# Kernel optimization log

Hardware: AMD Instinct MI355X
Metric: run time of the kernel (lower is better)

Reference implementation:

```python
import jax, jax.numpy as jnp
import numpy as np

B, L, S, H, E, D = 2, 2048, 2048, 8, 64, 64

def setup_inputs() -> dict:
    key = jax.random.key(0)
    kq, kk, kv = jax.random.split(key, 3)
    queries = jax.random.normal(kq, (B, L, H, E), dtype=jnp.float32)
    keys = jax.random.normal(kk, (B, S, H, E), dtype=jnp.float32)
    values = jax.random.normal(kv, (B, S, H, D), dtype=jnp.float32)
    return {"queries": queries, "keys": keys, "values": values}

def reference(queries, keys, values):
    # queries: [B,L,H,E], keys: [B,S,H,E], values: [B,S,H,D]
    E_ = queries.shape[-1]
    scale = 1.0 / jnp.sqrt(jnp.asarray(E_, dtype=queries.dtype))
    # scores: [B,H,L,S]
    scores = jnp.einsum('blhe,bshe->bhls', queries, keys)
    # mask_flag=False, use_relative_pos=False, dropout=0.0 -> identity
    A = jax.nn.softmax(scale * scores, axis=-1)
    # output: [B,L,H,D]
    V = jnp.einsum('bhls,bshd->blhd', A, values)
    return V
```

## Files before the change

kernel.cpp:

```cpp
#include <hip/hip_runtime.h>
#include <hip/hip_bf16.h>


#define LOG2E 1.44269504088896340736f
#define SCL2 0.18033688011112042f

#if __has_builtin(__builtin_amdgcn_exp2f)
#define EXP2(x) __builtin_amdgcn_exp2f(x)
#else
#define EXP2(x) exp2f(x)
#endif

typedef __attribute__((ext_vector_type(8))) short bf16x8;
typedef __attribute__((ext_vector_type(4))) float f32x4;
typedef __attribute__((ext_vector_type(16))) float f32x16;

static constexpr int Bc = 2, Lc = 2048, Sc = 2048, Hc = 8, Ec = 64, Dc = 64;
static constexpr int BH = Bc * Hc;
static constexpr int ELEMS = Bc * Lc * Hc * Ec;

static __device__ __forceinline__ unsigned short bfb(float x) {
  union { __hip_bfloat16 h; unsigned short u; } c;
  c.h = __float2bfloat16(x);
  return c.u;
}
static __device__ __forceinline__ unsigned pkbf(float a, float b) {
  union { __hip_bfloat162 h; unsigned u; } c;
  c.h = __float22bfloat162_rn(make_float2(a, b));
  return c.u;
}
static __device__ __forceinline__ bf16x8 pack4(unsigned w0, unsigned w1,
                                               unsigned w2, unsigned w3) {
  union { unsigned u[4]; bf16x8 v; } c;
  c.u[0] = w0; c.u[1] = w1; c.u[2] = w2; c.u[3] = w3;
  return c.v;
}

static __device__ __forceinline__ void plswap(unsigned a, unsigned b,
                                              unsigned& o0, unsigned& o1, int hi) {
#if __has_builtin(__builtin_amdgcn_permlane32_swap)
  auto r = __builtin_amdgcn_permlane32_swap(a, b, false, false);
  o0 = r[0];
  o1 = r[1];
#else
  unsigned ax = (unsigned)__shfl_xor((int)a, 32);
  unsigned bx = (unsigned)__shfl_xor((int)b, 32);
  o0 = hi ? bx : a;
  o1 = hi ? b : ax;
#endif
}
static __device__ __forceinline__ float cross_half_max(float x, int hi) {
  unsigned ua, ub;
  plswap(__float_as_uint(x), __float_as_uint(x), ua, ub, hi);
  return fmaxf(__uint_as_float(ua), __uint_as_float(ub));
}
static __device__ __forceinline__ float cross_half_sum(float x, int hi) {
  unsigned ua, ub;
  plswap(__float_as_uint(x), __float_as_uint(x), ua, ub, hi);
  return __uint_as_float(ua) + __uint_as_float(ub);
}

__global__ __launch_bounds__(256) void prep_kv_kernel(const float* __restrict__ K,
                                                      const float* __restrict__ V,
                                                      __hip_bfloat16* __restrict__ Kc,
                                                      __hip_bfloat16* __restrict__ Vt) {
  __shared__ __hip_bfloat16 tile[4][64][68];
  if (blockIdx.x < 1024) {
    int t = blockIdx.x * 256 + threadIdx.x;
    int f = t * 8;
    int e = f & 63;
    int h = (f >> 6) & 7;
    int s = (f >> 9) & 2047;
    int b = f >> 20;
    float4 v0 = *reinterpret_cast<const float4*>(K + f);
    float4 v1 = *reinterpret_cast<const float4*>(K + f + 4);
    int es = e >> 4, hi = (e >> 3) & 1;
    int kb = s >> 5, qi = s & 31;
    int o = ((b << 3) + h) * (Sc * 64) + kb * 2048 + es * 512 + hi * 256 + qi * 8;
    union { ushort u[8]; uint4 q; } pk;
    pk.u[0] = bfb(v0.x); pk.u[1] = bfb(v0.y); pk.u[2] = bfb(v0.z); pk.u[3] = bfb(v0.w);
    pk.u[4] = bfb(v1.x); pk.u[5] = bfb(v1.y); pk.u[6] = bfb(v1.z); pk.u[7] = bfb(v1.w);
    *reinterpret_cast<uint4*>(Kc + o) = pk.q;
  } else {
    const int w = threadIdx.x >> 6;
    const int lane = threadIdx.x & 63;
    const int task = (blockIdx.x - 1024) * 4 + w;
    const int st = task & 31;
    const int bh = task >> 5;
    const int s0 = st * 64;
    const int b = bh >> 3, h = bh & 7;
#pragma unroll 4
    for (int j = 0; j < 64; ++j) {
      float v = V[((b * Sc + s0 + j) * Hc + h) * 64 + lane];
      tile[w][j][lane] = __float2bfloat16(v);
    }
    __syncthreads();
    const int qi = lane & 31, hi = lane >> 5;
    __hip_bfloat16* Vb = Vt + bh * (Sc * 64);
#pragma unroll
    for (int kb2 = 0; kb2 < 2; ++kb2)
#pragma unroll
      for (int d0 = 0; d0 < 2; ++d0)
#pragma unroll
        for (int ks = 0; ks < 2; ++ks) {
          union { ushort u[8]; uint4 q; } pk;
#pragma unroll
          for (int j = 0; j < 8; ++j) {
            union { __hip_bfloat16 h; ushort u; } c;
            c.h = tile[w][kb2 * 32 + ks * 16 + hi * 8 + j][d0 * 32 + qi];
            pk.u[j] = c.u;
          }
          int o = ((s0 >> 5) + kb2) * 2048 + d0 * 1024 + ks * 512 + lane * 8;
          *reinterpret_cast<uint4*>(Vb + o) = pk.q;
        }
  }
}

static __device__ __forceinline__ void sm_group(f32x16& sc, float& m, float& l,
                                                f32x16& oA, f32x16& oB, int hi,
                                                bf16x8& pb0, bf16x8& pb1) {
  float x0 = fmaxf(fmaxf(sc[0], sc[1]), fmaxf(sc[2], sc[3]));
  float x1 = fmaxf(fmaxf(sc[4], sc[5]), fmaxf(sc[6], sc[7]));
  float x2 = fmaxf(fmaxf(sc[8], sc[9]), fmaxf(sc[10], sc[11]));
  float x3 = fmaxf(fmaxf(sc[12], sc[13]), fmaxf(sc[14], sc[15]));
  float mx = fmaxf(fmaxf(x0, x1), fmaxf(x2, x3));

  if (__any(mx > m + 64.0f)) {
    float mrow = cross_half_max(mx, hi);
    float mnew = fmaxf(m, mrow);
    float corr = EXP2((m - mnew) * SCL2);
    l *= corr;
#pragma unroll
    for (int r = 0; r < 16; ++r) { oA[r] *= corr; oB[r] *= corr; }
    m = mnew;
  }
  float mL = m * SCL2;
#pragma unroll
  for (int r = 0; r < 16; ++r) sc[r] = EXP2(sc[r] * SCL2 - mL);

  float r0 = (sc[0] + sc[1]) + (sc[2] + sc[3]);
  float r1 = (sc[4] + sc[5]) + (sc[6] + sc[7]);
  float r2 = (sc[8] + sc[9]) + (sc[10] + sc[11]);
  float r3 = (sc[12] + sc[13]) + (sc[14] + sc[15]);
  l += (r0 + r1) + (r2 + r3);

  unsigned c0, c1, c2, c3, y0, y1, y2, y3;
  c0 = pkbf(sc[0], sc[1]);  c1 = pkbf(sc[4], sc[5]);
  c2 = pkbf(sc[2], sc[3]);  c3 = pkbf(sc[6], sc[7]);
  plswap(c0, c1, y0, y2, hi);
  plswap(c2, c3, y1, y3, hi);
  pb0 = pack4(y0, y1, y2, y3);
  c0 = pkbf(sc[8], sc[9]);   c1 = pkbf(sc[12], sc[13]);
  c2 = pkbf(sc[10], sc[11]); c3 = pkbf(sc[14], sc[15]);
  plswap(c0, c1, y0, y2, hi);
  plswap(c2, c3, y1, y3, hi);
  pb1 = pack4(y0, y1, y2, y3);
}

__global__ __launch_bounds__(256, 2) void attn_kernel(const float* __restrict__ Qf,
                                                      const __hip_bfloat16* __restrict__ Kc,
                                                      const __hip_bfloat16* __restrict__ Vt,
                                                      float* __restrict__ Out) {
  __shared__ float obuf[4][2][16][64];
  __shared__ float mlb[2][4][2][32];

  const int lid = blockIdx.x;
  const int xcd = lid & 7;
  const int i = lid >> 3;
  const int bh = (xcd << 1) | (i >> 5);
  const int q0 = (i & 31) << 6;
  const int w = threadIdx.x >> 6;
  const int lane = threadIdx.x & 63;
  const int qi = lane & 31;
  const int hi = lane >> 5;
  const int b = bh >> 3, h = bh & 7;

  const __hip_bfloat16* Kh = Kc + bh * (Sc * 64);
  const __hip_bfloat16* Vh = Vt + bh * (Sc * 64);

  bf16x8 qf[2][4];
#pragma unroll
  for (int g = 0; g < 2; ++g) {
    const float* qrow = Qf + ((b * Lc + q0 + g * 32 + qi) * Hc + h) * 64 + hi * 8;
#pragma unroll
    for (int es = 0; es < 4; ++es) {
      float4 a = *reinterpret_cast<const float4*>(qrow + es * 16);
      float4 c = *reinterpret_cast<const float4*>(qrow + es * 16 + 4);
      qf[g][es] = pack4(pkbf(a.x, a.y), pkbf(a.z, a.w), pkbf(c.x, c.y), pkbf(c.z, c.w));
    }
  }

  f32x16 zero;
#pragma unroll
  for (int r = 0; r < 16; ++r) zero[r] = 0.f;

  f32x16 oa0 = zero, ob0 = zero, oa1 = zero, ob1 = zero;
  float m0 = -1.0e30f, l0 = 0.f, m1 = -1.0e30f, l1 = 0.f;

  bf16x8 kA0, kA1, kA2, kA3, vA0, vA1, vA2, vA3;
  bf16x8 kB0, kB1, kB2, kB3, vB0, vB1, vB2, vB3;

  auto loadKV = [&](bf16x8& k0, bf16x8& k1, bf16x8& k2, bf16x8& k3,
                    bf16x8& v0, bf16x8& v1, bf16x8& v2, bf16x8& v3, int s) {
    const __hip_bfloat16* Kp = Kh + (s >> 5) * 2048 + lane * 8;
    k0 = *reinterpret_cast<const bf16x8*>(Kp + 0 * 512);
    k1 = *reinterpret_cast<const bf16x8*>(Kp + 1 * 512);
    k2 = *reinterpret_cast<const bf16x8*>(Kp + 2 * 512);
    k3 = *reinterpret_cast<const bf16x8*>(Kp + 3 * 512);
    const __hip_bfloat16* Vp = Vh + (s >> 5) * 2048 + lane * 8;
    v0 = *reinterpret_cast<const bf16x8*>(Vp + 0 * 512);
    v1 = *reinterpret_cast<const bf16x8*>(Vp + 1 * 512);
    v2 = *reinterpret_cast<const bf16x8*>(Vp + 2 * 512);
    v3 = *reinterpret_cast<const bf16x8*>(Vp + 3 * 512);
  };

  auto compute = [&](bf16x8 k0, bf16x8 k1, bf16x8 k2, bf16x8 k3,
                     bf16x8 v0, bf16x8 v1, bf16x8 v2, bf16x8 v3) {
    f32x16 sc0, sc1;
    __builtin_amdgcn_s_setprio(1);
    sc0 = __builtin_amdgcn_mfma_f32_32x32x16_bf16(k0, qf[0][0], zero, 0, 0, 0);
    sc0 = __builtin_amdgcn_mfma_f32_32x32x16_bf16(k1, qf[0][1], sc0, 0, 0, 0);
    sc0 = __builtin_amdgcn_mfma_f32_32x32x16_bf16(k2, qf[0][2], sc0, 0, 0, 0);
    sc0 = __builtin_amdgcn_mfma_f32_32x32x16_bf16(k3, qf[0][3], sc0, 0, 0, 0);
    sc1 = __builtin_amdgcn_mfma_f32_32x32x16_bf16(k0, qf[1][0], zero, 0, 0, 0);
    sc1 = __builtin_amdgcn_mfma_f32_32x32x16_bf16(k1, qf[1][1], sc1, 0, 0, 0);
    sc1 = __builtin_amdgcn_mfma_f32_32x32x16_bf16(k2, qf[1][2], sc1, 0, 0, 0);
    sc1 = __builtin_amdgcn_mfma_f32_32x32x16_bf16(k3, qf[1][3], sc1, 0, 0, 0);
    __builtin_amdgcn_s_setprio(0);

    bf16x8 pb0, pb1;
    sm_group(sc0, m0, l0, oa0, ob0, hi, pb0, pb1);
    __builtin_amdgcn_s_setprio(1);
    oa0 = __builtin_amdgcn_mfma_f32_32x32x16_bf16(v0, pb0, oa0, 0, 0, 0);
    oa0 = __builtin_amdgcn_mfma_f32_32x32x16_bf16(v1, pb1, oa0, 0, 0, 0);
    ob0 = __builtin_amdgcn_mfma_f32_32x32x16_bf16(v2, pb0, ob0, 0, 0, 0);
    ob0 = __builtin_amdgcn_mfma_f32_32x32x16_bf16(v3, pb1, ob0, 0, 0, 0);
    __builtin_amdgcn_s_setprio(0);

    sm_group(sc1, m1, l1, oa1, ob1, hi, pb0, pb1);
    __builtin_amdgcn_s_setprio(1);
    oa1 = __builtin_amdgcn_mfma_f32_32x32x16_bf16(v0, pb0, oa1, 0, 0, 0);
    oa1 = __builtin_amdgcn_mfma_f32_32x32x16_bf16(v1, pb1, oa1, 0, 0, 0);
    ob1 = __builtin_amdgcn_mfma_f32_32x32x16_bf16(v2, pb0, ob1, 0, 0, 0);
    ob1 = __builtin_amdgcn_mfma_f32_32x32x16_bf16(v3, pb1, ob1, 0, 0, 0);
    __builtin_amdgcn_s_setprio(0);
  };

  loadKV(kA0, kA1, kA2, kA3, vA0, vA1, vA2, vA3, w * 32);
  for (int s = w * 32; s < Sc; s += 256) {
    loadKV(kB0, kB1, kB2, kB3, vB0, vB1, vB2, vB3, s + 128);
    compute(kA0, kA1, kA2, kA3, vA0, vA1, vA2, vA3);
    if (s + 256 < Sc)
      loadKV(kA0, kA1, kA2, kA3, vA0, vA1, vA2, vA3, s + 256);
    compute(kB0, kB1, kB2, kB3, vB0, vB1, vB2, vB3);
  }

  l0 = cross_half_sum(l0, hi);
  l1 = cross_half_sum(l1, hi);

  if (hi == 0) {
    mlb[0][w][0][qi] = m0; mlb[0][w][1][qi] = l0;
    mlb[1][w][0][qi] = m1; mlb[1][w][1][qi] = l1;
  }
  __syncthreads();
  float myf[2], inv[2];
#pragma unroll
  for (int g = 0; g < 2; ++g) {
    float mm = fmaxf(fmaxf(mlb[g][0][0][qi], mlb[g][1][0][qi]),
                     fmaxf(mlb[g][2][0][qi], mlb[g][3][0][qi]));
    float Lt = 0.f;
#pragma unroll
    for (int sw = 0; sw < 4; ++sw)
      Lt += EXP2((mlb[g][sw][0][qi] - mm) * SCL2) * mlb[g][sw][1][qi];
    float mreg = g ? m1 : m0;
    myf[g] = EXP2((mreg - mm) * SCL2);
    inv[g] = 1.0f / Lt;
  }
  const int d0 = w >> 1, rr = (w & 1) * 8;
#pragma unroll
  for (int g = 0; g < 2; ++g) {
    if (g) __syncthreads();
    const f32x16& A = g ? oa1 : oa0;
    const f32x16& Bv = g ? ob1 : ob0;
#pragma unroll
    for (int r = 0; r < 16; ++r) {
      obuf[w][0][r][lane] = A[r] * myf[g];
      obuf[w][1][r][lane] = Bv[r] * myf[g];
    }
    __syncthreads();
    float* orow = Out + ((b * Lc + q0 + g * 32 + qi) * Hc + h) * Dc;
#pragma unroll
    for (int t = 0; t < 2; ++t) {
      f32x4 acc;
#pragma unroll
      for (int j = 0; j < 4; ++j) {
        const int r = rr + 4 * t + j;
        acc[j] = (obuf[0][d0][r][lane] + obuf[1][d0][r][lane] +
                  obuf[2][d0][r][lane] + obuf[3][d0][r][lane]) * inv[g];
      }
      const int dbase = d0 * 32 + ((rr + 4 * t) >> 2) * 8 + hi * 4;
      *reinterpret_cast<f32x4*>(orow + dbase) = acc;
    }
  }
}

extern "C" void kernel_launch(void* const* d_in, const int* in_sizes, int n_in,
                              void* d_out, int out_size, void* d_ws, size_t ws_size,
                              hipStream_t stream) {
  const float* Q = (const float*)d_in[0];
  const float* K = (const float*)d_in[1];
  const float* V = (const float*)d_in[2];
  float* out = (float*)d_out;

  __hip_bfloat16* Kc = (__hip_bfloat16*)d_ws;
  __hip_bfloat16* Vt = Kc + ELEMS;

  prep_kv_kernel<<<dim3(1152), 256, 0, stream>>>(K, V, Kc, Vt);
  attn_kernel<<<dim3(512), 256, 0, stream>>>(Q, Kc, Vt, out);
}
```

Baseline: 43.81 us.

## Stage K/V tiles into LDS via direct global_load_lds double buffering

Replaces register-based K/V prefetching with asynchronous global-to-LDS direct loads into a per-wave double buffer, then reads fragments from LDS before MFMA. This aims to cut VGPR pressure and VMEM latency exposure while overlapping the next tile's load with compute. The shared buffer is unioned with the output reduction buffer, which raises LDS use to about 64 KB per block and adds an LDS read round-trip plus a full vmcnt wait each iteration.

```diff
diff --git a/kernel.cpp b/kernel.cpp
--- a/kernel.cpp
+++ b/kernel.cpp
@@ -58,6 +58,12 @@
   unsigned ua, ub;
   plswap(__float_as_uint(x), __float_as_uint(x), ua, ub, hi);
   return __uint_as_float(ua) + __uint_as_float(ub);
+}
+
+static __device__ __forceinline__ void gld16(const __hip_bfloat16* g, __hip_bfloat16* l) {
+  __builtin_amdgcn_global_load_lds(
+      (const __attribute__((address_space(1))) void*)g,
+      (__attribute__((address_space(3))) void*)l, 16, 0, 0);
 }
 
 __global__ __launch_bounds__(256) void prep_kv_kernel(const float* __restrict__ K,
@@ -161,7 +167,11 @@
                                                       const __hip_bfloat16* __restrict__ Kc,
                                                       const __hip_bfloat16* __restrict__ Vt,
                                                       float* __restrict__ Out) {
-  __shared__ float obuf[4][2][16][64];
+  union SMem {
+    __hip_bfloat16 kv[4][2][4096];
+    float obuf[4][2][16][64];
+  };
+  __shared__ SMem sm;
   __shared__ float mlb[2][4][2][32];
 
   const int lid = blockIdx.x;
@@ -178,6 +188,16 @@
   const __hip_bfloat16* Kh = Kc + bh * (Sc * 64);
   const __hip_bfloat16* Vh = Vt + bh * (Sc * 64);
 
+  auto stage = [&](int t, int c) {
+    const int tb = (w + 4 * t) * 2048;
+    const __hip_bfloat16* Ks = Kh + tb + lane * 8;
+    const __hip_bfloat16* Vs = Vh + tb + lane * 8;
+#pragma unroll
+    for (int f = 0; f < 4; ++f) gld16(Ks + f * 512, &sm.kv[w][c][f * 512]);
+#pragma unroll
+    for (int f = 0; f < 4; ++f) gld16(Vs + f * 512, &sm.kv[w][c][2048 + f * 512]);
+  };
+
   bf16x8 qf[2][4];
 #pragma unroll
   for (int g = 0; g < 2; ++g) {
@@ -197,25 +217,25 @@
   f32x16 oa0 = zero, ob0 = zero, oa1 = zero, ob1 = zero;
   float m0 = -1.0e30f, l0 = 0.f, m1 = -1.0e30f, l1 = 0.f;
 
-  bf16x8 kA0, kA1, kA2, kA3, vA0, vA1, vA2, vA3;
-  bf16x8 kB0, kB1, kB2, kB3, vB0, vB1, vB2, vB3;
-
-  auto loadKV = [&](bf16x8& k0, bf16x8& k1, bf16x8& k2, bf16x8& k3,
-                    bf16x8& v0, bf16x8& v1, bf16x8& v2, bf16x8& v3, int s) {
-    const __hip_bfloat16* Kp = Kh + (s >> 5) * 2048 + lane * 8;
-    k0 = *reinterpret_cast<const bf16x8*>(Kp + 0 * 512);
-    k1 = *reinterpret_cast<const bf16x8*>(Kp + 1 * 512);
-    k2 = *reinterpret_cast<const bf16x8*>(Kp + 2 * 512);
-    k3 = *reinterpret_cast<const bf16x8*>(Kp + 3 * 512);
-    const __hip_bfloat16* Vp = Vh + (s >> 5) * 2048 + lane * 8;
-    v0 = *reinterpret_cast<const bf16x8*>(Vp + 0 * 512);
-    v1 = *reinterpret_cast<const bf16x8*>(Vp + 1 * 512);
-    v2 = *reinterpret_cast<const bf16x8*>(Vp + 2 * 512);
-    v3 = *reinterpret_cast<const bf16x8*>(Vp + 3 * 512);
-  };
-
-  auto compute = [&](bf16x8 k0, bf16x8 k1, bf16x8 k2, bf16x8 k3,
-                     bf16x8 v0, bf16x8 v1, bf16x8 v2, bf16x8 v3) {
+  stage(0, 0);
+  int cur = 0;
+
+  for (int t = 0; t < 16; ++t) {
+    asm volatile("s_waitcnt vmcnt(0)" ::: "memory");
+    __builtin_amdgcn_sched_barrier(0);
+
+    const __hip_bfloat16* kb = &sm.kv[w][cur][lane * 8];
+    bf16x8 k0 = *reinterpret_cast<const bf16x8*>(kb + 0 * 512);
+    bf16x8 k1 = *reinterpret_cast<const bf16x8*>(kb + 1 * 512);
+    bf16x8 k2 = *reinterpret_cast<const bf16x8*>(kb + 2 * 512);
+    bf16x8 k3 = *reinterpret_cast<const bf16x8*>(kb + 3 * 512);
+    bf16x8 v0 = *reinterpret_cast<const bf16x8*>(kb + 4 * 512);
+    bf16x8 v1 = *reinterpret_cast<const bf16x8*>(kb + 5 * 512);
+    bf16x8 v2 = *reinterpret_cast<const bf16x8*>(kb + 6 * 512);
+    bf16x8 v3 = *reinterpret_cast<const bf16x8*>(kb + 7 * 512);
+
+    if (t + 1 < 16) stage(t + 1, cur ^ 1);
+
     f32x16 sc0, sc1;
     __builtin_amdgcn_s_setprio(1);
     sc0 = __builtin_amdgcn_mfma_f32_32x32x16_bf16(k0, qf[0][0], zero, 0, 0, 0);
@@ -244,15 +264,8 @@
     ob1 = __builtin_amdgcn_mfma_f32_32x32x16_bf16(v2, pb0, ob1, 0, 0, 0);
     ob1 = __builtin_amdgcn_mfma_f32_32x32x16_bf16(v3, pb1, ob1, 0, 0, 0);
     __builtin_amdgcn_s_setprio(0);
-  };
-
-  loadKV(kA0, kA1, kA2, kA3, vA0, vA1, vA2, vA3, w * 32);
-  for (int s = w * 32; s < Sc; s += 256) {
-    loadKV(kB0, kB1, kB2, kB3, vB0, vB1, vB2, vB3, s + 128);
-    compute(kA0, kA1, kA2, kA3, vA0, vA1, vA2, vA3);
-    if (s + 256 < Sc)
-      loadKV(kA0, kA1, kA2, kA3, vA0, vA1, vA2, vA3, s + 256);
-    compute(kB0, kB1, kB2, kB3, vB0, vB1, vB2, vB3);
+
+    cur ^= 1;
   }
 
   l0 = cross_half_sum(l0, hi);
@@ -284,8 +297,8 @@
     const f32x16& Bv = g ? ob1 : ob0;
 #pragma unroll
     for (int r = 0; r < 16; ++r) {
-      obuf[w][0][r][lane] = A[r] * myf[g];
-      obuf[w][1][r][lane] = Bv[r] * myf[g];
+      sm.obuf[w][0][r][lane] = A[r] * myf[g];
+      sm.obuf[w][1][r][lane] = Bv[r] * myf[g];
     }
     __syncthreads();
     float* orow = Out + ((b * Lc + q0 + g * 32 + qi) * Hc + h) * Dc;
@@ -295,8 +308,8 @@
 #pragma unroll
       for (int j = 0; j < 4; ++j) {
         const int r = rr + 4 * t + j;
-        acc[j] = (obuf[0][d0][r][lane] + obuf[1][d0][r][lane] +
-                  obuf[2][d0][r][lane] + obuf[3][d0][r][lane]) * inv[g];
+        acc[j] = (sm.obuf[0][d0][r][lane] + sm.obuf[1][d0][r][lane] +
+                  sm.obuf[2][d0][r][lane] + sm.obuf[3][d0][r][lane]) * inv[g];
       }
       const int dbase = d0 * 32 + ((rr + 4 * t) >> 2) * 8 + hi * 4;
       *reinterpret_cast<f32x4*>(orow + dbase) = acc;
```

After: 46.37 us. 5.8% more time.
